# Performance work log

Measured on AMD Instinct MI355X. Metric: run time of the kernel, lower is better.

Reference implementation:

```python
import jax, jax.numpy as jnp
import numpy as np

N_NODES = 100000
N_EDGES = 1600000
D_IN = 128
D_HID = 64


def setup_inputs() -> dict:
    key = jax.random.key(0)
    k1, k2, k3, k4 = jax.random.split(key, 4)
    x = jax.random.normal(k1, (N_NODES, D_IN), dtype=jnp.float32)
    edge_index = jax.random.randint(k2, (2, N_EDGES), 0, N_NODES, dtype=jnp.int64)
    W1 = jax.random.normal(k3, (D_IN, D_HID), dtype=jnp.float32) / np.sqrt(D_IN)
    b1 = jnp.zeros((D_HID,), dtype=jnp.float32)
    W2 = jax.random.normal(k4, (D_HID, 1), dtype=jnp.float32) / np.sqrt(D_HID)
    b2 = jnp.zeros((1,), dtype=jnp.float32)
    return {"x": x, "edge_index": edge_index, "W1": W1, "b1": b1, "W2": W2, "b2": b2}


def _gcn_layer(x, W, b, src, dst, norm, n):
    # PyG GCNConv: linear transform, then normalized scatter-add aggregation, then bias
    h = x @ W                                   # [N, d_out]
    msg = h[src] * norm[:, None]                # gather + edge-weight   [E', d_out]
    out = jax.ops.segment_sum(msg, dst, num_segments=n)  # scatter-add
    return out + b


def reference(x, edge_index, W1, b1, W2, b2):
    n = x.shape[0]
    loops = jnp.arange(n, dtype=edge_index.dtype)
    src = jnp.concatenate([edge_index[0], loops])  # self-loops added (GCN default)
    dst = jnp.concatenate([edge_index[1], loops])
    # symmetric normalization: deg^{-1/2}[src] * deg^{-1/2}[dst]
    deg = jax.ops.segment_sum(jnp.ones(dst.shape, x.dtype), dst, num_segments=n)
    dis = jnp.where(deg > 0, jax.lax.rsqrt(jnp.maximum(deg, 1e-12)), 0.0)
    norm = dis[src] * dis[dst]
    h = jax.nn.relu(_gcn_layer(x, W1, b1, src, dst, norm, n))
    y = _gcn_layer(h, W2, b2, src, dst, norm, n)   # [N, 1]
    # ConstantPad1d((0, num_node_features-1), 0) -> [N, D_IN]
    return jnp.pad(y, ((0, 0), (0, x.shape[1] - 1)))
```

## Files before the change

kernel.cpp:

```cpp
#include <hip/hip_runtime.h>

#define N_NODES 100000
#define N_EDGES 1600000
#define D_IN 128
#define D_HID 64

#define BKT_SHIFT 8
#define BKT_NODES 256
#define NB 391
#define NBLK 392
#define SLOT 32
#define SEG4 (SLOT / 4)
#define REG4 (NBLK * SEG4)
#define BKT_CAP 5120
#define OVF_CAP 8192

#define EST 512
#define BST 1024

typedef __attribute__((ext_vector_type(8))) short bf16x8;
typedef __attribute__((ext_vector_type(4))) float f32x4;

__device__ __forceinline__ unsigned short f2b(float f) {
    union { float f; unsigned u; } c; c.f = f;
    unsigned r = (c.u + 0x7FFFu + ((c.u >> 16) & 1u)) >> 16;
    return (unsigned short)r;
}
__device__ __forceinline__ float blo(unsigned u) { return __uint_as_float(u << 16); }
__device__ __forceinline__ float bhi(unsigned u) { return __uint_as_float(u & 0xffff0000u); }

__global__ __launch_bounds__(256) void k_prep(const float* __restrict__ W1,
                                              unsigned short* __restrict__ w1t,
                                              int* __restrict__ ovf_cnt) {
    int t = blockIdx.x * 256 + threadIdx.x;
    if (t == 0) ovf_cnt[0] = 0;
    int k = t >> 6, f = t & 63;
    w1t[f * D_IN + k] = f2b(W1[t]);
}

__global__ __launch_bounds__(EST) void k_escatter(const int* __restrict__ src,
                                                  const int* __restrict__ dst,
                                                  int* __restrict__ pairs,
                                                  int* __restrict__ cnt_blk,
                                                  int* __restrict__ ovf_cnt,
                                                  int2* __restrict__ ovf, int E) {
    __shared__ int lcur[NB];
    __shared__ int lp[NB * SLOT];
    int tid = threadIdx.x;
    for (int t = tid; t < NB; t += EST) lcur[t] = 0;
    __syncthreads();
    int chunk = (E + NBLK - 1) / NBLK;
    int beg = blockIdx.x * chunk;
    int end = min(beg + chunk, E);
    for (int e = beg + tid; e < end; e += EST) {
        int d = dst[e], s = src[e];
        int bk = d >> BKT_SHIFT;
        int slot = atomicAdd(&lcur[bk], 1);
        if (slot < SLOT)
            lp[(bk << 5) + slot] = (s << BKT_SHIFT) | (d & (BKT_NODES - 1));
        else {
            int o = atomicAdd(ovf_cnt, 1);
            if (o < OVF_CAP) ovf[o] = make_int2(s, d);
        }
    }
    __syncthreads();
    uint4* p4 = (uint4*)pairs;
    const uint4* lp4 = (const uint4*)lp;
    for (int i4 = tid; i4 < NB * SEG4; i4 += EST) {
        int bk = i4 >> 3;
        int c = min(lcur[bk], SLOT);
        if (((i4 & 7) << 2) < c)
            p4[((size_t)bk * NBLK + blockIdx.x) * SEG4 + (i4 & 7)] = lp4[i4];
    }
    for (int t = tid; t < NB; t += EST)
        cnt_blk[t * NBLK + blockIdx.x] = min(lcur[t], SLOT);
}

__global__ __launch_bounds__(BST) void k_bsort(const uint4* __restrict__ pairs4,
                                               const int* __restrict__ cnt_blk,
                                               const int* __restrict__ ovf_cnt,
                                               const int2* __restrict__ ovf,
                                               int* __restrict__ srcs_sorted,
                                               int* __restrict__ row_start,
                                               int* __restrict__ row_end,
                                               float* __restrict__ dis, int n) {
    __shared__ uint4 reg4[REG4];
    __shared__ int segc[NBLK];
    __shared__ int cnt[BKT_NODES];
    __shared__ int exc[BKT_NODES];
    __shared__ int sorted[BKT_CAP];
    __shared__ int nE_sh;
    int b = blockIdx.x;
    int tid = threadIdx.x;
    int node0 = b << BKT_SHIFT;
    int ocnt = min(ovf_cnt[0], OVF_CAP);
    const uint4* region = pairs4 + (size_t)b * REG4;

    for (int i = tid; i < NBLK; i += BST) segc[i] = cnt_blk[b * NBLK + i];
    if (tid < BKT_NODES) cnt[tid] = 0;
    __syncthreads();

    for (int i4 = tid; i4 < REG4; i4 += BST) {
        int c = segc[i4 >> 3];
        int k = (i4 & 7) * 4;
        if (k < c) {
            uint4 v = region[i4];
            reg4[i4] = v;
            atomicAdd(&cnt[v.x & (BKT_NODES - 1)], 1);
            if (k + 1 < c) atomicAdd(&cnt[v.y & (BKT_NODES - 1)], 1);
            if (k + 2 < c) atomicAdd(&cnt[v.z & (BKT_NODES - 1)], 1);
            if (k + 3 < c) atomicAdd(&cnt[v.w & (BKT_NODES - 1)], 1);
        }
    }
    for (int k = tid; k < ocnt; k += BST) {
        int2 e = ovf[k];
        if ((e.y >> BKT_SHIFT) == b) atomicAdd(&cnt[e.y & (BKT_NODES - 1)], 1);
    }
    __syncthreads();

    if (tid < 64) {
        int run = 0;
        for (int c = 0; c < BKT_NODES; c += 64) {
            int v = cnt[c + tid];
            int inc = v;
            for (int off = 1; off < 64; off <<= 1) {
                int t2 = __shfl_up(inc, off);
                if (tid >= off) inc += t2;
            }
            exc[c + tid] = run + inc - v;
            run += __shfl(inc, 63);
        }
        if (tid == 63) nE_sh = run;
    }
    __syncthreads();

    if (tid < BKT_NODES) {
        int node = node0 + tid;
        if (node < n) {
            int rs = b * BKT_CAP + exc[tid];
            row_start[node] = rs;
            row_end[node] = rs + cnt[tid];
            dis[node] = rsqrtf((float)cnt[tid] + 1.0f);
        }
    }
    int nE = nE_sh;
    __syncthreads();
    if (tid < BKT_NODES) cnt[tid] = exc[tid];
    __syncthreads();

    for (int i4 = tid; i4 < REG4; i4 += BST) {
        int c = segc[i4 >> 3];
        int k = (i4 & 7) * 4;
        if (k < c) {
            uint4 v = reg4[i4];
            { int p = atomicAdd(&cnt[v.x & (BKT_NODES - 1)], 1); sorted[p] = (int)(v.x >> 8); }
            if (k + 1 < c) { int p = atomicAdd(&cnt[v.y & (BKT_NODES - 1)], 1); sorted[p] = (int)(v.y >> 8); }
            if (k + 2 < c) { int p = atomicAdd(&cnt[v.z & (BKT_NODES - 1)], 1); sorted[p] = (int)(v.z >> 8); }
            if (k + 3 < c) { int p = atomicAdd(&cnt[v.w & (BKT_NODES - 1)], 1); sorted[p] = (int)(v.w >> 8); }
        }
    }
    for (int k = tid; k < ocnt; k += BST) {
        int2 e = ovf[k];
        if ((e.y >> BKT_SHIFT) == b) {
            int p = atomicAdd(&cnt[e.y & (BKT_NODES - 1)], 1);
            sorted[p] = e.x;
        }
    }
    __syncthreads();

    int gbase = b * BKT_CAP;
    for (int k = tid; k < nE; k += BST)
        srcs_sorted[gbase + k] = sorted[k];
}

#define LS 136
__global__ __launch_bounds__(256) void k_gemm1(const float* __restrict__ x,
                                               const uint4* __restrict__ w1t4,
                                               const float* __restrict__ dis,
                                               unsigned short* __restrict__ h1s, int n) {
    __shared__ unsigned short xs[64 * LS];
    __shared__ unsigned short ws[64 * LS];
    int tid = threadIdx.x;
    int node0 = blockIdx.x * 64;

#pragma unroll
    for (int it = 0; it < 4; ++it) {
        int e = tid + it * 256;
        int f = e >> 4, c = e & 15;
        *(uint4*)&ws[f * LS + c * 8] = w1t4[e];
    }
#pragma unroll
    for (int it = 0; it < 8; ++it) {
        int e4 = tid + it * 256;
        int node = e4 >> 5;
        int k = (e4 & 31) * 4;
        float4 v = make_float4(0.f, 0.f, 0.f, 0.f);
        if (node0 + node < n)
            v = ((const float4*)x)[((size_t)(node0 + node) * D_IN + k) >> 2];
        uint2 u;
        u.x = (unsigned)f2b(v.x) | ((unsigned)f2b(v.y) << 16);
        u.y = (unsigned)f2b(v.z) | ((unsigned)f2b(v.w) << 16);
        *(uint2*)&xs[node * LS + k] = u;
    }
    __syncthreads();

    int wv = tid >> 6;
    int lane = tid & 63;
    int m16 = lane & 15;
    int q = lane >> 4;

    bf16x8 afrag[4];
#pragma unroll
    for (int ks = 0; ks < 4; ++ks)
        afrag[ks] = *(const bf16x8*)&xs[(wv * 16 + m16) * LS + ks * 32 + q * 8];

    f32x4 acc[4];
#pragma unroll
    for (int ft = 0; ft < 4; ++ft) acc[ft] = (f32x4){0.f, 0.f, 0.f, 0.f};

#pragma unroll
    for (int ft = 0; ft < 4; ++ft)
#pragma unroll
        for (int ks = 0; ks < 4; ++ks) {
            bf16x8 bfrag = *(const bf16x8*)&ws[(ft * 16 + m16) * LS + ks * 32 + q * 8];
            acc[ft] = __builtin_amdgcn_mfma_f32_16x16x32_bf16(afrag[ks], bfrag, acc[ft], 0, 0, 0);
        }

#pragma unroll
    for (int r = 0; r < 4; ++r) {
        int node = node0 + wv * 16 + q * 4 + r;
        if (node < n) {
            float d = dis[node];
#pragma unroll
            for (int ft = 0; ft < 4; ++ft)
                h1s[(size_t)node * D_HID + ft * 16 + m16] = f2b(acc[ft][r] * d);
        }
    }
}

__global__ __launch_bounds__(256) void k_gather1(const int* __restrict__ srcs,
                                                 const int* __restrict__ row_start,
                                                 const int* __restrict__ row_end,
                                                 const float* __restrict__ dis,
                                                 const uint4* __restrict__ h4,
                                                 const float* __restrict__ b1,
                                                 const float* __restrict__ W2,
                                                 float* __restrict__ zd, int n) {
    int i = blockIdx.x * 8 + (threadIdx.x >> 5);
    int lane = threadIdx.x & 63;
    int g = (lane >> 3) & 3;
    int m8 = lane & 7;
    float dd = dis[i];

    float a0, a1, a2, a3, a4, a5, a6, a7;
    {
        uint4 u = h4[(unsigned)i * 8u + m8];
        float w = (g == 0) ? 1.f : 0.f;
        a0 = w * blo(u.x); a1 = w * bhi(u.x);
        a2 = w * blo(u.y); a3 = w * bhi(u.y);
        a4 = w * blo(u.z); a5 = w * bhi(u.z);
        a6 = w * blo(u.w); a7 = w * bhi(u.w);
    }

#define ACC(u) { a0 += blo(u.x); a1 += bhi(u.x); a2 += blo(u.y); a3 += bhi(u.y); \
                 a4 += blo(u.z); a5 += bhi(u.z); a6 += blo(u.w); a7 += bhi(u.w); }
    int end = row_end[i];
    int j = row_start[i] + g;
    for (; j + 12 < end; j += 16) {
        int s0 = srcs[j];
        int s1 = srcs[j + 4];
        int s2 = srcs[j + 8];
        int s3 = srcs[j + 12];
        uint4 u0 = h4[(unsigned)s0 * 8u + m8];
        uint4 u1 = h4[(unsigned)s1 * 8u + m8];
        uint4 u2 = h4[(unsigned)s2 * 8u + m8];
        uint4 u3 = h4[(unsigned)s3 * 8u + m8];
        ACC(u0); ACC(u1); ACC(u2); ACC(u3);
    }
    for (; j + 4 < end; j += 8) {
        int s0 = srcs[j];
        int s1 = srcs[j + 4];
        uint4 u0 = h4[(unsigned)s0 * 8u + m8];
        uint4 u1 = h4[(unsigned)s1 * 8u + m8];
        ACC(u0); ACC(u1);
    }
    if (j < end) {
        int s0 = srcs[j];
        uint4 u0 = h4[(unsigned)s0 * 8u + m8];
        ACC(u0);
    }
#undef ACC

#pragma unroll
    for (int off = 8; off < 32; off <<= 1) {
        a0 += __shfl_xor(a0, off); a1 += __shfl_xor(a1, off);
        a2 += __shfl_xor(a2, off); a3 += __shfl_xor(a3, off);
        a4 += __shfl_xor(a4, off); a5 += __shfl_xor(a5, off);
        a6 += __shfl_xor(a6, off); a7 += __shfl_xor(a7, off);
    }
    float4 ba = ((const float4*)b1)[m8 * 2];
    float4 bb = ((const float4*)b1)[m8 * 2 + 1];
    float4 wa = ((const float4*)W2)[m8 * 2];
    float4 wb = ((const float4*)W2)[m8 * 2 + 1];
    float v = fmaxf(fmaf(dd, a0, ba.x), 0.f) * wa.x + fmaxf(fmaf(dd, a1, ba.y), 0.f) * wa.y
            + fmaxf(fmaf(dd, a2, ba.z), 0.f) * wa.z + fmaxf(fmaf(dd, a3, ba.w), 0.f) * wa.w
            + fmaxf(fmaf(dd, a4, bb.x), 0.f) * wb.x + fmaxf(fmaf(dd, a5, bb.y), 0.f) * wb.y
            + fmaxf(fmaf(dd, a6, bb.z), 0.f) * wb.z + fmaxf(fmaf(dd, a7, bb.w), 0.f) * wb.w;
#pragma unroll
    for (int off = 1; off < 8; off <<= 1) v += __shfl_xor(v, off);
    if ((lane & 31) == 0) zd[i] = v * dd;
}

__global__ __launch_bounds__(256) void k_gather2(const int* __restrict__ srcs,
                                                 const int* __restrict__ row_start,
                                                 const int* __restrict__ row_end,
                                                 const float* __restrict__ dis,
                                                 const float* __restrict__ zd,
                                                 const float* __restrict__ b2,
                                                 float* __restrict__ out, int n) {
    int i = blockIdx.x * 8 + (threadIdx.x >> 5);
    int l = threadIdx.x & 31;
    float acc = 0.f;
    int beg = row_start[i], end = row_end[i];
    for (int j = beg + l; j < end; j += 32)
        acc += zd[srcs[j]];
#pragma unroll
    for (int off = 1; off < 32; off <<= 1) acc += __shfl_xor(acc, off);
    float y = (acc + zd[i]) * dis[i] + b2[0];
    float4 v = make_float4(0.f, 0.f, 0.f, 0.f);
    if (l == 0) v.x = y;
    ((float4*)out)[(size_t)i * 32 + l] = v;
}

extern "C" void kernel_launch(void* const* d_in, const int* in_sizes, int n_in,
                              void* d_out, int out_size, void* d_ws, size_t ws_size,
                              hipStream_t stream) {
    const float* x  = (const float*)d_in[0];
    const int*   ei = (const int*)d_in[1];
    const float* W1 = (const float*)d_in[2];
    const float* b1 = (const float*)d_in[3];
    const float* W2 = (const float*)d_in[4];
    const float* b2 = (const float*)d_in[5];
    float* out = (float*)d_out;

    const int n = N_NODES;
    const int E = N_EDGES;
    const int* src = ei;
    const int* dst = ei + E;

    int* pairs       = (int*)d_ws;
    int* cnt_blk     = pairs + (size_t)NB * NBLK * SLOT;
    int* srcs_sorted = cnt_blk + (size_t)NB * NBLK;
    int* row_start   = srcs_sorted + (size_t)NB * BKT_CAP;
    int* row_end     = row_start + n;
    int* ovf_cnt     = row_end + n;
    int2* ovf        = (int2*)(ovf_cnt + 4);
    float* dis       = (float*)(ovf + OVF_CAP);
    unsigned short* h1s = (unsigned short*)(dis + n);
    unsigned short* w1t = h1s + (size_t)n * D_HID;
    float* zd        = (float*)(w1t + D_IN * D_HID);

    k_prep<<<32, 256, 0, stream>>>(W1, w1t, ovf_cnt);
    k_escatter<<<NBLK, EST, 0, stream>>>(src, dst, pairs, cnt_blk, ovf_cnt, ovf, E);
    k_bsort<<<NB, BST, 0, stream>>>((const uint4*)pairs, cnt_blk, ovf_cnt, ovf,
                                    srcs_sorted, row_start, row_end, dis, n);

    k_gemm1<<<(n + 63) / 64, 256, 0, stream>>>(x, (const uint4*)w1t, dis, h1s, n);

    k_gather1<<<(n + 7) / 8, 256, 0, stream>>>(srcs_sorted, row_start, row_end, dis,
                                               (const uint4*)h1s, b1, W2, zd, n);
    k_gather2<<<(n + 7) / 8, 256, 0, stream>>>(srcs_sorted, row_start, row_end, dis,
                                               zd, b2, out, n);
}
```

Before: 195.3 us.

## Drop prep kernel, stage GEMM output via LDS, split gather1 launch

Removes the k_prep kernel: W1 is now converted to bf16 and transposed inside every k_gemm1 block, and the overflow counter is cleared with a memset. k_escatter writes full fixed-size slot segments without checking counts, and k_gemm1 stages its output tile in shared memory so it can write it out as coalesced 16-byte stores. gather1 is split into two launches over node halves. This saves one launch and improves store coalescing, but each GEMM block now does redundant W1 conversion with scattered 2-byte LDS writes, and it writes unused pair slots.

Result: slower. 203.4 us (+4.1%).

```diff
diff --git a/kernel.cpp b/kernel.cpp
--- a/kernel.cpp
+++ b/kernel.cpp
@@ -28,15 +28,6 @@
 }
 __device__ __forceinline__ float blo(unsigned u) { return __uint_as_float(u << 16); }
 __device__ __forceinline__ float bhi(unsigned u) { return __uint_as_float(u & 0xffff0000u); }
-
-__global__ __launch_bounds__(256) void k_prep(const float* __restrict__ W1,
-                                              unsigned short* __restrict__ w1t,
-                                              int* __restrict__ ovf_cnt) {
-    int t = blockIdx.x * 256 + threadIdx.x;
-    if (t == 0) ovf_cnt[0] = 0;
-    int k = t >> 6, f = t & 63;
-    w1t[f * D_IN + k] = f2b(W1[t]);
-}
 
 __global__ __launch_bounds__(EST) void k_escatter(const int* __restrict__ src,
                                                   const int* __restrict__ dst,
@@ -66,12 +57,8 @@
     __syncthreads();
     uint4* p4 = (uint4*)pairs;
     const uint4* lp4 = (const uint4*)lp;
-    for (int i4 = tid; i4 < NB * SEG4; i4 += EST) {
-        int bk = i4 >> 3;
-        int c = min(lcur[bk], SLOT);
-        if (((i4 & 7) << 2) < c)
-            p4[((size_t)bk * NBLK + blockIdx.x) * SEG4 + (i4 & 7)] = lp4[i4];
-    }
+    for (int i4 = tid; i4 < NB * SEG4; i4 += EST)
+        p4[((size_t)(i4 >> 3) * NBLK + blockIdx.x) * SEG4 + (i4 & 7)] = lp4[i4];
     for (int t = tid; t < NB; t += EST)
         cnt_blk[t * NBLK + blockIdx.x] = min(lcur[t], SLOT);
 }
@@ -175,7 +162,7 @@
 
 #define LS 136
 __global__ __launch_bounds__(256) void k_gemm1(const float* __restrict__ x,
-                                               const uint4* __restrict__ w1t4,
+                                               const float* __restrict__ W1,
                                                const float* __restrict__ dis,
                                                unsigned short* __restrict__ h1s, int n) {
     __shared__ unsigned short xs[64 * LS];
@@ -184,10 +171,10 @@
     int node0 = blockIdx.x * 64;
 
 #pragma unroll
-    for (int it = 0; it < 4; ++it) {
+    for (int it = 0; it < 32; ++it) {
         int e = tid + it * 256;
-        int f = e >> 4, c = e & 15;
-        *(uint4*)&ws[f * LS + c * 8] = w1t4[e];
+        int k = e >> 6, f = e & 63;
+        ws[f * LS + k] = f2b(W1[e]);
     }
 #pragma unroll
     for (int it = 0; it < 8; ++it) {
@@ -226,15 +213,25 @@
             acc[ft] = __builtin_amdgcn_mfma_f32_16x16x32_bf16(afrag[ks], bfrag, acc[ft], 0, 0, 0);
         }
 
+    __syncthreads();
+    unsigned short* hs = xs;
 #pragma unroll
     for (int r = 0; r < 4; ++r) {
-        int node = node0 + wv * 16 + q * 4 + r;
-        if (node < n) {
-            float d = dis[node];
-#pragma unroll
-            for (int ft = 0; ft < 4; ++ft)
-                h1s[(size_t)node * D_HID + ft * 16 + m16] = f2b(acc[ft][r] * d);
-        }
+        int nl = wv * 16 + q * 4 + r;
+        int node = node0 + nl;
+        float d = (node < n) ? dis[node] : 0.f;
+#pragma unroll
+        for (int ft = 0; ft < 4; ++ft)
+            hs[nl * 64 + ft * 16 + m16] = f2b(acc[ft][r] * d);
+    }
+    __syncthreads();
+
+    const uint4* hs4 = (const uint4*)hs;
+    uint4* h14 = (uint4*)h1s;
+#pragma unroll
+    for (int i = tid; i < 512; i += 256) {
+        int node = node0 + (i >> 3);
+        if (node < n) h14[(size_t)node * 8 + (i & 7)] = hs4[i];
     }
 }
 
@@ -245,8 +242,8 @@
                                                  const uint4* __restrict__ h4,
                                                  const float* __restrict__ b1,
                                                  const float* __restrict__ W2,
-                                                 float* __restrict__ zd, int n) {
-    int i = blockIdx.x * 8 + (threadIdx.x >> 5);
+                                                 float* __restrict__ zd, int i0) {
+    int i = i0 + blockIdx.x * 8 + (threadIdx.x >> 5);
     int lane = threadIdx.x & 63;
     int g = (lane >> 3) & 3;
     int m8 = lane & 7;
@@ -357,18 +354,19 @@
     int2* ovf        = (int2*)(ovf_cnt + 4);
     float* dis       = (float*)(ovf + OVF_CAP);
     unsigned short* h1s = (unsigned short*)(dis + n);
-    unsigned short* w1t = h1s + (size_t)n * D_HID;
-    float* zd        = (float*)(w1t + D_IN * D_HID);
-
-    k_prep<<<32, 256, 0, stream>>>(W1, w1t, ovf_cnt);
+    float* zd        = (float*)(h1s + (size_t)n * D_HID);
+
+    hipMemsetAsync(ovf_cnt, 0, sizeof(int), stream);
     k_escatter<<<NBLK, EST, 0, stream>>>(src, dst, pairs, cnt_blk, ovf_cnt, ovf, E);
     k_bsort<<<NB, BST, 0, stream>>>((const uint4*)pairs, cnt_blk, ovf_cnt, ovf,
                                     srcs_sorted, row_start, row_end, dis, n);
 
-    k_gemm1<<<(n + 63) / 64, 256, 0, stream>>>(x, (const uint4*)w1t, dis, h1s, n);
-
-    k_gather1<<<(n + 7) / 8, 256, 0, stream>>>(srcs_sorted, row_start, row_end, dis,
-                                               (const uint4*)h1s, b1, W2, zd, n);
+    k_gemm1<<<(n + 63) / 64, 256, 0, stream>>>(x, W1, dis, h1s, n);
+
+    k_gather1<<<6250, 256, 0, stream>>>(srcs_sorted, row_start, row_end, dis,
+                                        (const uint4*)h1s, b1, W2, zd, 0);
+    k_gather1<<<6250, 256, 0, stream>>>(srcs_sorted, row_start, row_end, dis,
+                                        (const uint4*)h1s, b1, W2, zd, 50000);
     k_gather2<<<(n + 7) / 8, 256, 0, stream>>>(srcs_sorted, row_start, row_end, dis,
                                                zd, b2, out, n);
 }
```
